# Kernel tuning notes

Hardware: AMD Instinct MI355X
Metric: run time of the kernel (lower is better)

## Reference

```python
import jax, jax.numpy as jnp
import numpy as np

D_MODEL = 1024
HEADS = 16
D_K = D_MODEL // HEADS
THETA = 10000.0


def _rope(x, pos):
    # x: [B, H, S, d_k]; pos: [S]
    half = D_K // 2
    inv_freq = 1.0 / (THETA ** (jnp.arange(0, D_K, 2, dtype=jnp.float32) / D_K))  # [half]
    ang = pos.astype(jnp.float32)[:, None] * inv_freq[None, :]  # [S, half]
    cos, sin = jnp.cos(ang), jnp.sin(ang)
    x1 = x[..., 0::2]  # even components
    x2 = x[..., 1::2]  # odd components
    o1 = x1 * cos - x2 * sin
    o2 = x1 * sin + x2 * cos
    # interleave back to original layout
    out = jnp.stack([o1, o2], axis=-1).reshape(x.shape)
    return out


def setup_inputs() -> dict:
    key = jax.random.key(0)
    ks = jax.random.split(key, 5)
    B, S = 4, 2048
    scale = 1.0 / np.sqrt(D_MODEL)
    return {
        "x": jax.random.normal(ks[0], (B, S, D_MODEL), dtype=jnp.float32),
        "Wq": jax.random.normal(ks[1], (D_MODEL, D_MODEL), dtype=jnp.float32) * scale,
        "Wk": jax.random.normal(ks[2], (D_MODEL, D_MODEL), dtype=jnp.float32) * scale,
        "Wv": jax.random.normal(ks[3], (D_MODEL, D_MODEL), dtype=jnp.float32) * scale,
        "Wo": jax.random.normal(ks[4], (D_MODEL, D_MODEL), dtype=jnp.float32) * scale,
    }


def reference(x, Wq, Wk, Wv, Wo):
    B, S, _ = x.shape
    # Linear weights are [out, in]; y = x @ W.T
    def proj(W):
        y = jnp.einsum('bsd,ed->bse', x, W)
        return y.reshape(B, S, HEADS, D_K).transpose(0, 2, 1, 3)  # [B,H,S,d_k]
    Q, K, V = proj(Wq), proj(Wk), proj(Wv)
    pos = jnp.arange(S, dtype=jnp.int32)
    Q = _rope(Q, pos)
    K = _rope(K, pos)
    scores = jnp.einsum('bhqd,bhkd->bhqk', Q, K) / jnp.sqrt(jnp.float32(D_K))
    causal = jnp.tril(jnp.ones((S, S), dtype=bool))
    scores = jnp.where(causal, scores, jnp.finfo(scores.dtype).min)
    attn = jax.nn.softmax(scores, axis=-1)
    mh = jnp.einsum('bhqk,bhkd->bhqd', attn, V)  # [B,H,S,d_v]
    mh = mh.transpose(0, 2, 1, 3).reshape(B, S, D_MODEL)
    return jnp.einsum('bsd,ed->bse', mh, Wo)
```

## Files before the change

### kernel.cpp

```cpp
#include <hip/hip_runtime.h>

typedef unsigned short u16;
typedef unsigned int   u32;
typedef __attribute__((ext_vector_type(8))) short s16x8;
typedef __attribute__((ext_vector_type(4))) float f32x4;
typedef __attribute__((ext_vector_type(16))) float f32x16;
typedef __attribute__((ext_vector_type(2))) int i32x2;

#define D_MODEL 1024
#define S_LEN   2048
#define BATCH   4
#define HEADS   16
#define DK      64
#define M_TOTAL (BATCH * S_LEN)

#define QSCALE 0.18033688011112042f
#define ROPE_L2 0.41524101186092029f

__device__ __forceinline__ u16 f2b(float f) {
  u32 u = __float_as_uint(f);
  u32 r = u + 0x7FFFu + ((u >> 16) & 1u);
  return (u16)(r >> 16);
}
__device__ __forceinline__ u32 packtrunc(float f0, float f1) {
  return (__float_as_uint(f0) >> 16) | (__float_as_uint(f1) & 0xFFFF0000u);
}
__device__ __forceinline__ u32 packrn(float f0, float f1) {
  return (u32)f2b(f0) | ((u32)f2b(f1) << 16);
}

extern "C" __device__ float __ocml_native_exp2_f32(float);
__device__ __forceinline__ float fexp2(float x) {
#if __has_builtin(__builtin_amdgcn_exp2f)
  return __builtin_amdgcn_exp2f(x);
#else
  return __ocml_native_exp2_f32(x);
#endif
}

template<int N> __device__ __forceinline__ void waitvm() {
  asm volatile("s_waitcnt vmcnt(%0)" :: "n"(N) : "memory");
}

typedef const __attribute__((address_space(1))) unsigned int* gas_u32p;
typedef __attribute__((address_space(3))) unsigned int* las_u32p;
#define GLL16(gp, lp) __builtin_amdgcn_global_load_lds((gas_u32p)(gp), (las_u32p)(lp), 16, 0, 0)

__global__ void k_cvt(const float* __restrict__ x,
                      const float* __restrict__ a, const float* __restrict__ b,
                      const float* __restrict__ c, const float* __restrict__ d,
                      u16* __restrict__ Xb, u16* __restrict__ Wb) {
  int i = blockIdx.x * blockDim.x + threadIdx.x;
  if (i < 2097152) {
    float4 v = ((const float4*)x)[i];
    ((u32*)Xb)[2 * i]     = packrn(v.x, v.y);
    ((u32*)Xb)[2 * i + 1] = packrn(v.z, v.w);
  } else {
    int j = i - 2097152;
    const float* src = (j < 524288) ? ((j < 262144) ? a : b) : ((j < 786432) ? c : d);
    float4 v = ((const float4*)src)[j & 0x3FFFF];
    ((u32*)Wb)[2 * j]     = packrn(v.x, v.y);
    ((u32*)Wb)[2 * j + 1] = packrn(v.z, v.w);
  }
}

template<int BM, int BN, bool BF16OUT, bool ROPE, bool DUAL>
__launch_bounds__(512, 2)
__global__ void k_gemm2(const u16* __restrict__ A, const u16* __restrict__ B,
                        void* __restrict__ C, void* __restrict__ C2,
                        int M, int N, int K, float scale) {
  constexpr int WM = BM / 2;
  constexpr int WN = BN / 4;
  constexpr int FM = WM / 16;
  constexpr int FN = WN / 16;
  constexpr int SA = BM / 128;
  constexpr int SB = BN / 128;
  constexpr int L  = SA + SB;
  constexpr int ASLOT = BM * 32;
  constexpr int SLOT  = (BM + BN) * 32;
  __shared__ u16 SH[4 * SLOT];

  const int tid  = threadIdx.x;
  const int lane = tid & 63;
  const int w    = tid >> 6;
  const int wm2  = w >> 2;
  const int wn2  = w & 3;
  const int rl   = lane & 15;
  const int q    = lane >> 4;
  const int bm = blockIdx.y * BM, bn = blockIdx.x * BN;

  const int rowS = tid >> 2;
  const int blkS = (tid & 3) ^ (rowS & 3);
  const u16* Asrc = A + (size_t)(bm + rowS) * K + blkS * 8;
  const u16* Bsrc = B + (size_t)(bn + rowS) * K + blkS * 8;
  const int dstL = w * 512;

  const int fbase = rl * 32 + ((q ^ (rl & 3)) * 8);
  const int abase = wm2 * WM * 32 + fbase;
  const int bbase = ASLOT + wn2 * WN * 32 + fbase;

  f32x4 acc[FM][FN];
#pragma unroll
  for (int i = 0; i < FM; i++)
#pragma unroll
    for (int j = 0; j < FN; j++) acc[i][j] = (f32x4){0.f, 0.f, 0.f, 0.f};

  const int nt = K >> 5;

  auto STAGE = [&](int t) {
    u16* slot = SH + (t & 3) * SLOT;
    const int k0 = t << 5;
#pragma unroll
    for (int s = 0; s < SA; s++)
      GLL16(Asrc + (size_t)(s * 128) * K + k0, slot + s * 4096 + dstL);
#pragma unroll
    for (int s = 0; s < SB; s++)
      GLL16(Bsrc + (size_t)(s * 128) * K + k0, slot + ASLOT + s * 4096 + dstL);
  };

  STAGE(0); STAGE(1); STAGE(2);

  for (int t = 0; t < nt; t++) {
    if (t < nt - 2)       waitvm<2 * L>();
    else if (t == nt - 2) waitvm<L>();
    else                  waitvm<0>();
    __builtin_amdgcn_s_barrier();

    const u16* slot = SH + (t & 3) * SLOT;
    s16x8 af[FM], bfr[FN];
#pragma unroll
    for (int mi = 0; mi < FM; mi++)
      af[mi] = *(const s16x8*)(slot + abase + mi * 512);
#pragma unroll
    for (int ni = 0; ni < FN; ni++)
      bfr[ni] = *(const s16x8*)(slot + bbase + ni * 512);

    if (t + 3 < nt) STAGE(t + 3);

    __builtin_amdgcn_s_setprio(1);
#pragma unroll
    for (int mi = 0; mi < FM; mi++)
#pragma unroll
      for (int ni = 0; ni < FN; ni++)
        acc[mi][ni] = __builtin_amdgcn_mfma_f32_16x16x32_bf16(af[mi], bfr[ni], acc[mi][ni], 0, 0, 0);
    __builtin_amdgcn_s_setprio(0);
  }

  const bool isQ = !DUAL || (bn < D_MODEL);
  u16* Cd = (u16*)(isQ ? C : C2);
  const int bnL = DUAL ? (bn & (D_MODEL - 1)) : bn;
  const float sc = isQ ? scale : 1.0f;

#pragma unroll
  for (int mi = 0; mi < FM; mi++)
#pragma unroll
    for (int ni = 0; ni < FN; ni++) {
      if (ROPE) {
        const int col = bnL + wn2 * WN + ni * 16 + rl;
        const int fi  = (col & 63) >> 1;
        const float inv = exp2f(-(float)fi * ROPE_L2);
        const bool odd = (rl & 1);
#pragma unroll
        for (int r = 0; r < 4; r++) {
          int grow = bm + wm2 * WM + mi * 16 + q * 4 + r;
          float own = acc[mi][ni][r];
          float oth = __shfl_xor(own, 1);
          float ang = (float)(grow & (S_LEN - 1)) * inv;
          float sn, cs;
          __sincosf(ang, &sn, &cs);
          float x1 = odd ? oth : own;
          float x2 = odd ? own : oth;
          float res = odd ? (x1 * sn + x2 * cs) : (x1 * cs - x2 * sn);
          acc[mi][ni][r] = res * sc;
        }
      }
#pragma unroll
      for (int r = 0; r < 4; r++) {
        int grow = bm + wm2 * WM + mi * 16 + q * 4 + r;
        int gcol = bnL + wn2 * WN + ni * 16 + rl;
        float v = acc[mi][ni][r];
        if (BF16OUT) Cd[(size_t)grow * N + gcol] = f2b(v);
        else         ((float*)Cd)[(size_t)grow * N + gcol] = v;
      }
    }
}

__launch_bounds__(256, 4)
__global__ void k_attn(const u16* __restrict__ Qb, const u16* __restrict__ Kb,
                       const u16* __restrict__ Vtg, u16* __restrict__ Mh) {
  __shared__ u16 SH[128 * 64 + 64 * 128];
  u16* Kl = SH;
  u16* Vt = SH + 128 * 64;
  const int tid  = threadIdx.x;
  const int lane = tid & 63;
  const int w    = tid >> 6;
  const int n    = lane & 31;
  const int h    = lane >> 5;
  const int nx   = n & 7;
  const int bid = blockIdx.x;
  const int r   = bid >> 3;
  const int u   = r & 15;
  const int bh  = (bid & 7) + 8 * (r >> 4);
  const int hd  = bh & 15, b = bh >> 4;
  const int s   = (w & 2) ? (62 - 2 * u + (w & 1)) : (2 * u + (w & 1));
  const int rb  = s * 32;
  const int ktiles = ((63 - 2 * u) >> 2) + 1;
  const size_t kbase = ((size_t)b * S_LEN) * D_MODEL + (size_t)hd * DK;
  const size_t vbase = ((size_t)hd * DK) * M_TOTAL + (size_t)b * S_LEN;

  const int hx    = ((h ^ nx) << 3);
  const int kidx0 = n * 64  + hx;
  const int vidx0 = n * 128 + hx;

  s16x8 bq[4];
#pragma unroll
  for (int ks = 0; ks < 4; ks++)
    bq[ks] = *(const s16x8*)(Qb + kbase + (size_t)(rb + n) * D_MODEL + ks * 16 + h * 8);

  f32x16 o[2];
#pragma unroll
  for (int dt = 0; dt < 2; dt++)
#pragma unroll
    for (int i = 0; i < 16; i++) o[dt][i] = 0.f;
  float psum = 0.f;

  const int krow_l = lane >> 3;
  const int kblk_l = (lane & 7) ^ krow_l;
  const u16* KgL = Kb + kbase + (size_t)(w * 32 + krow_l) * D_MODEL + kblk_l * 8;
  u16* KdL = Kl + (w * 32) * 64;
  const int vrow_l = lane >> 4;
  const int vblk_l = lane & 15;
  const u16* VgL = Vtg + vbase + (size_t)(w * 16 + vrow_l) * M_TOTAL;
  u16* VdL = Vt + (w * 16) * 128;

  for (int t = 0; t < ktiles; t++) {
    const int k0 = t * 128;
    __syncthreads();
#pragma unroll
    for (int i = 0; i < 4; i++)
      GLL16(KgL + (size_t)(k0 + i * 8) * D_MODEL, KdL + i * 8 * 64);
#pragma unroll
    for (int i = 0; i < 4; i++) {
      const int jj = vblk_l ^ ((i * 4 + vrow_l) & 7);
      GLL16(VgL + (size_t)(i * 4) * M_TOTAL + k0 + jj * 8, VdL + i * 4 * 128);
    }
    __syncthreads();

#pragma unroll
    for (int kt = 0; kt < 4; kt++) {
      const int k0t = k0 + kt * 32;
      if (k0t > rb + 31) continue;

      s16x8 ak[4], vf[4];
#pragma unroll
      for (int ks = 0; ks < 4; ks++)
        ak[ks] = *(const s16x8*)(Kl + ((kidx0 ^ (ks << 4)) + kt * 2048));
#pragma unroll
      for (int c = 0; c < 2; c++)
#pragma unroll
        for (int dt = 0; dt < 2; dt++)
          vf[c * 2 + dt] = *(const s16x8*)(Vt + ((vidx0 ^ (kt * 32 + c * 16)) + dt * 4096));

      f32x16 Sc;
#pragma unroll
      for (int i = 0; i < 16; i++) Sc[i] = 0.f;
#pragma unroll
      for (int ks = 0; ks < 4; ks++)
        Sc = __builtin_amdgcn_mfma_f32_32x32x16_bf16(ak[ks], bq[ks], Sc, 0, 0, 0);

      u32 P0[4], P1[4];
      float ps01 = 0.f, ps23 = 0.f;
      if ((k0t + 31) > rb) {
        const int lim = rb + n - k0t - 4 * h;
#pragma unroll
        for (int g = 0; g < 4; g++) {
          float pv[4];
#pragma unroll
          for (int t2 = 0; t2 < 4; t2++) {
            float e = fexp2(Sc[4 * g + t2]);
            pv[t2] = (8 * g + t2 <= lim) ? e : 0.f;
          }
          ps01 += pv[0] + pv[1];
          ps23 += pv[2] + pv[3];
          P0[g] = packtrunc(pv[0], pv[1]);
          P1[g] = packtrunc(pv[2], pv[3]);
        }
      } else {
#pragma unroll
        for (int g = 0; g < 4; g++) {
          float pv[4];
#pragma unroll
          for (int t2 = 0; t2 < 4; t2++) pv[t2] = fexp2(Sc[4 * g + t2]);
          ps01 += pv[0] + pv[1];
          ps23 += pv[2] + pv[3];
          P0[g] = packtrunc(pv[0], pv[1]);
          P1[g] = packtrunc(pv[2], pv[3]);
        }
      }
      psum += ps01 + ps23;

#pragma unroll
      for (int c = 0; c < 2; c++) {
        i32x2 rA = __builtin_amdgcn_permlane32_swap((int)P0[2 * c], (int)P0[2 * c + 1], false, false);
        i32x2 rB = __builtin_amdgcn_permlane32_swap((int)P1[2 * c], (int)P1[2 * c + 1], false, false);
        union { u32 uu[4]; s16x8 v; } pb;
        pb.uu[0] = (u32)rA[0];
        pb.uu[1] = (u32)rB[0];
        pb.uu[2] = (u32)rA[1];
        pb.uu[3] = (u32)rB[1];
        o[0] = __builtin_amdgcn_mfma_f32_32x32x16_bf16(vf[c * 2 + 0], pb.v, o[0], 0, 0, 0);
        o[1] = __builtin_amdgcn_mfma_f32_32x32x16_bf16(vf[c * 2 + 1], pb.v, o[1], 0, 0, 0);
      }
    }
  }

  float l = psum + __shfl_xor(psum, 32);
  const float linv = 1.0f / l;
  __syncthreads();
  u16* Olw = SH + w * 32 * 66;
#pragma unroll
  for (int dt = 0; dt < 2; dt++) {
#pragma unroll
    for (int g = 0; g < 4; g++) {
      u32 lo = packrn(o[dt][4 * g + 0] * linv, o[dt][4 * g + 1] * linv);
      u32 hi = packrn(o[dt][4 * g + 2] * linv, o[dt][4 * g + 3] * linv);
      *(uint2*)(Olw + n * 66 + dt * 32 + 8 * g + 4 * h) = (uint2){lo, hi};
    }
  }
  const int rr = lane >> 3, seg = lane & 7;
#pragma unroll
  for (int ro = 0; ro < 32; ro += 8) {
    uint4 v = *(const uint4*)(Olw + (ro + rr) * 66 + seg * 8);
    *(uint4*)(Mh + ((size_t)b * S_LEN + rb + ro + rr) * D_MODEL + hd * DK + seg * 8) = v;
  }
}

extern "C" void kernel_launch(void* const* d_in, const int* in_sizes, int n_in,
                              void* d_out, int out_size, void* d_ws, size_t ws_size,
                              hipStream_t stream) {
  const float* x  = (const float*)d_in[0];
  const float* Wq = (const float*)d_in[1];
  const float* Wk = (const float*)d_in[2];
  const float* Wv = (const float*)d_in[3];
  const float* Wo = (const float*)d_in[4];
  float* out = (float*)d_out;

  char* ws = (char*)d_ws;
  const size_t xsz = (size_t)M_TOTAL * D_MODEL * 2;
  const size_t wsz = (size_t)D_MODEL * D_MODEL * 2;
  u16* Xb  = (u16*)ws; ws += xsz;
  u16* Wqb = (u16*)ws; ws += wsz;
  u16* Wkb = (u16*)ws; ws += wsz;
  u16* Wvb = (u16*)ws; ws += wsz;
  u16* Wob = (u16*)ws; ws += wsz;
  u16* Qb  = (u16*)ws; ws += xsz;
  u16* Kb  = (u16*)ws; ws += xsz;
  u16* Vtg = (u16*)ws; ws += xsz;
  u16* Mh  = (u16*)ws; ws += xsz;

  k_cvt<<<12288, 256, 0, stream>>>(x, Wq, Wk, Wv, Wo, Xb, Wqb);

  k_gemm2<256, 256, true, true, true><<<dim3(8, 32), 512, 0, stream>>>(
      Xb, Wqb, Qb, Kb, M_TOTAL, D_MODEL, D_MODEL, QSCALE);
  k_gemm2<128, 256, true, false, false><<<dim3(32, 8), 512, 0, stream>>>(
      Wvb, Xb, Vtg, Vtg, D_MODEL, M_TOTAL, D_MODEL, 1.0f);

  k_attn<<<dim3(1024), 256, 0, stream>>>(Qb, Kb, Vtg, Mh);

  k_gemm2<256, 128, false, false, false><<<dim3(8, 32), 512, 0, stream>>>(
      Mh, Wob, out, out, M_TOTAL, D_MODEL, D_MODEL, 1.0f);
}
```

Before: 254.7 us.

## Replace GEMM kernel with 128x128 tiles, triple-buffered LDS and grouped block remap

```diff
diff --git a/kernel.cpp b/kernel.cpp
--- a/kernel.cpp
+++ b/kernel.cpp
@@ -40,6 +40,12 @@
 
 template<int N> __device__ __forceinline__ void waitvm() {
   asm volatile("s_waitcnt vmcnt(%0)" :: "n"(N) : "memory");
+}
+
+template<int OFF> __device__ __forceinline__ s16x8 ldsr(unsigned a) {
+  s16x8 r;
+  asm volatile("ds_read_b128 %0, %1 offset:%2" : "=v"(r) : "v"(a), "n"(OFF));
+  return r;
 }
 
 typedef const __attribute__((address_space(1))) unsigned int* gas_u32p;
@@ -64,86 +70,83 @@
   }
 }
 
-template<int BM, int BN, bool BF16OUT, bool ROPE, bool DUAL>
-__launch_bounds__(512, 2)
-__global__ void k_gemm2(const u16* __restrict__ A, const u16* __restrict__ B,
+template<int GX, bool BF16OUT, bool ROPE, bool DUAL>
+__launch_bounds__(256, 3)
+__global__ void k_gemm3(const u16* __restrict__ A, const u16* __restrict__ B,
                         void* __restrict__ C, void* __restrict__ C2,
-                        int M, int N, int K, float scale) {
-  constexpr int WM = BM / 2;
-  constexpr int WN = BN / 4;
-  constexpr int FM = WM / 16;
-  constexpr int FN = WN / 16;
-  constexpr int SA = BM / 128;
-  constexpr int SB = BN / 128;
-  constexpr int L  = SA + SB;
-  constexpr int ASLOT = BM * 32;
-  constexpr int SLOT  = (BM + BN) * 32;
-  __shared__ u16 SH[4 * SLOT];
-
+                        int N, int K, float scale) {
+  constexpr int SLOT = 8192;
+  __shared__ u16 SH[3 * SLOT];
   const int tid  = threadIdx.x;
   const int lane = tid & 63;
   const int w    = tid >> 6;
-  const int wm2  = w >> 2;
-  const int wn2  = w & 3;
-  const int rl   = lane & 15;
-  const int q    = lane >> 4;
-  const int bm = blockIdx.y * BM, bn = blockIdx.x * BN;
+  const int wm2  = w >> 1, wn2 = w & 1;
+  const int rl   = lane & 15, q = lane >> 4;
+
+  const int nwg = gridDim.x;
+  const int bid = (blockIdx.x & 7) * (nwg >> 3) + (blockIdx.x >> 3);
+  const int bx = bid % GX, by = bid / GX;
+  const int bm = by * 128, bn = bx * 128;
 
   const int rowS = tid >> 2;
   const int blkS = (tid & 3) ^ (rowS & 3);
   const u16* Asrc = A + (size_t)(bm + rowS) * K + blkS * 8;
   const u16* Bsrc = B + (size_t)(bn + rowS) * K + blkS * 8;
-  const int dstL = w * 512;
-
+
+  const unsigned shb = (unsigned)(size_t)(las_u32p)SH;
   const int fbase = rl * 32 + ((q ^ (rl & 3)) * 8);
-  const int abase = wm2 * WM * 32 + fbase;
-  const int bbase = ASLOT + wn2 * WN * 32 + fbase;
-
-  f32x4 acc[FM][FN];
-#pragma unroll
-  for (int i = 0; i < FM; i++)
-#pragma unroll
-    for (int j = 0; j < FN; j++) acc[i][j] = (f32x4){0.f, 0.f, 0.f, 0.f};
+  unsigned aR = shb + 2 * (wm2 * 2048 + fbase);
+  unsigned bR = shb + 2 * (4096 + wn2 * 2048 + fbase);
+
+  f32x4 acc[4][4];
+#pragma unroll
+  for (int i = 0; i < 4; i++)
+#pragma unroll
+    for (int j = 0; j < 4; j++) acc[i][j] = (f32x4){0.f, 0.f, 0.f, 0.f};
 
   const int nt = K >> 5;
 
-  auto STAGE = [&](int t) {
-    u16* slot = SH + (t & 3) * SLOT;
+  auto stage = [&](int t, int eoff) {
     const int k0 = t << 5;
-#pragma unroll
-    for (int s = 0; s < SA; s++)
-      GLL16(Asrc + (size_t)(s * 128) * K + k0, slot + s * 4096 + dstL);
-#pragma unroll
-    for (int s = 0; s < SB; s++)
-      GLL16(Bsrc + (size_t)(s * 128) * K + k0, slot + ASLOT + s * 4096 + dstL);
+    u16* d = SH + eoff + w * 512;
+#pragma unroll
+    for (int s2 = 0; s2 < 2; s2++) {
+      GLL16(Asrc + (size_t)(s2 * 64) * K + k0, d + s2 * 2048);
+      GLL16(Bsrc + (size_t)(s2 * 64) * K + k0, d + 4096 + s2 * 2048);
+    }
   };
 
-  STAGE(0); STAGE(1); STAGE(2);
+  stage(0, 0);
+  stage(1, SLOT);
+  int pslot = 2 * SLOT;
 
   for (int t = 0; t < nt; t++) {
-    if (t < nt - 2)       waitvm<2 * L>();
-    else if (t == nt - 2) waitvm<L>();
-    else                  waitvm<0>();
+    if (t < nt - 1) waitvm<4>();
+    else            waitvm<0>();
     __builtin_amdgcn_s_barrier();
 
-    const u16* slot = SH + (t & 3) * SLOT;
-    s16x8 af[FM], bfr[FN];
-#pragma unroll
-    for (int mi = 0; mi < FM; mi++)
-      af[mi] = *(const s16x8*)(slot + abase + mi * 512);
-#pragma unroll
-    for (int ni = 0; ni < FN; ni++)
-      bfr[ni] = *(const s16x8*)(slot + bbase + ni * 512);
-
-    if (t + 3 < nt) STAGE(t + 3);
+    s16x8 af[4], bf[4];
+    af[0] = ldsr<0>(aR);  af[1] = ldsr<1024>(aR);
+    af[2] = ldsr<2048>(aR); af[3] = ldsr<3072>(aR);
+    bf[0] = ldsr<0>(bR);  bf[1] = ldsr<1024>(bR);
+    bf[2] = ldsr<2048>(bR); bf[3] = ldsr<3072>(bR);
+
+    if (t + 2 < nt) stage(t + 2, pslot);
+
+    asm volatile("s_waitcnt lgkmcnt(0)" ::: "memory");
+    __builtin_amdgcn_sched_barrier(0);
 
     __builtin_amdgcn_s_setprio(1);
 #pragma unroll
-    for (int mi = 0; mi < FM; mi++)
-#pragma unroll
-      for (int ni = 0; ni < FN; ni++)
-        acc[mi][ni] = __builtin_amdgcn_mfma_f32_16x16x32_bf16(af[mi], bfr[ni], acc[mi][ni], 0, 0, 0);
+    for (int mi = 0; mi < 4; mi++)
+#pragma unroll
+      for (int ni = 0; ni < 4; ni++)
+        acc[mi][ni] = __builtin_amdgcn_mfma_f32_16x16x32_bf16(af[mi], bf[ni], acc[mi][ni], 0, 0, 0);
     __builtin_amdgcn_s_setprio(0);
+
+    aR = (aR >= shb + 2 * 2 * SLOT) ? aR - 2 * 2 * SLOT : aR + 2 * SLOT;
+    bR = (bR >= shb + 2 * 2 * SLOT + 8192) ? bR - 2 * 2 * SLOT : bR + 2 * SLOT;
+    pslot = (pslot == 2 * SLOT) ? 0 : pslot + SLOT;
   }
 
   const bool isQ = !DUAL || (bn < D_MODEL);
@@ -152,17 +155,17 @@
   const float sc = isQ ? scale : 1.0f;
 
 #pragma unroll
-  for (int mi = 0; mi < FM; mi++)
-#pragma unroll
-    for (int ni = 0; ni < FN; ni++) {
+  for (int mi = 0; mi < 4; mi++)
+#pragma unroll
+    for (int ni = 0; ni < 4; ni++) {
       if (ROPE) {
-        const int col = bnL + wn2 * WN + ni * 16 + rl;
+        const int col = bnL + wn2 * 64 + ni * 16 + rl;
         const int fi  = (col & 63) >> 1;
         const float inv = exp2f(-(float)fi * ROPE_L2);
         const bool odd = (rl & 1);
 #pragma unroll
         for (int r = 0; r < 4; r++) {
-          int grow = bm + wm2 * WM + mi * 16 + q * 4 + r;
+          int grow = bm + wm2 * 64 + mi * 16 + q * 4 + r;
           float own = acc[mi][ni][r];
           float oth = __shfl_xor(own, 1);
           float ang = (float)(grow & (S_LEN - 1)) * inv;
@@ -176,8 +179,8 @@
       }
 #pragma unroll
       for (int r = 0; r < 4; r++) {
-        int grow = bm + wm2 * WM + mi * 16 + q * 4 + r;
-        int gcol = bnL + wn2 * WN + ni * 16 + rl;
+        int grow = bm + wm2 * 64 + mi * 16 + q * 4 + r;
+        int gcol = bnL + wn2 * 64 + ni * 16 + rl;
         float v = acc[mi][ni][r];
         if (BF16OUT) Cd[(size_t)grow * N + gcol] = f2b(v);
         else         ((float*)Cd)[(size_t)grow * N + gcol] = v;
@@ -360,13 +363,13 @@
 
   k_cvt<<<12288, 256, 0, stream>>>(x, Wq, Wk, Wv, Wo, Xb, Wqb);
 
-  k_gemm2<256, 256, true, true, true><<<dim3(8, 32), 512, 0, stream>>>(
-      Xb, Wqb, Qb, Kb, M_TOTAL, D_MODEL, D_MODEL, QSCALE);
-  k_gemm2<128, 256, true, false, false><<<dim3(32, 8), 512, 0, stream>>>(
-      Wvb, Xb, Vtg, Vtg, D_MODEL, M_TOTAL, D_MODEL, 1.0f);
+  k_gemm3<16, true, true, true><<<1024, 256, 0, stream>>>(
+      Xb, Wqb, Qb, Kb, D_MODEL, D_MODEL, QSCALE);
+  k_gemm3<64, true, false, false><<<512, 256, 0, stream>>>(
+      Wvb, Xb, Vtg, Vtg, M_TOTAL, D_MODEL, 1.0f);
 
   k_attn<<<dim3(1024), 256, 0, stream>>>(Qb, Kb, Vtg, Mh);
 
-  k_gemm2<256, 128, false, false, false><<<dim3(8, 32), 512, 0, stream>>>(
-      Mh, Wob, out, out, M_TOTAL, D_MODEL, D_MODEL, 1.0f);
-}
+  k_gemm3<8, false, false, false><<<512, 256, 0, stream>>>(
+      Mh, Wob, out, out, D_MODEL, D_MODEL, 1.0f);
+}
```

Measured after the change: 245.1 us. -3.8%, faster.
